# Optimization experiments

Measured on AMD Instinct MI355X. Metric: run time of the kernel, lower is better.

## Reference

```python
import jax, jax.numpy as jnp
import numpy as np

N = 20000
E = 320000
D = 512
H = 512


def _gcn_norm(edge_index, num_nodes):
    # PyG GCNConv: add self-loops, then sym-normalize with in-degree of A+I
    src = jnp.concatenate([edge_index[0], jnp.arange(num_nodes)])
    dst = jnp.concatenate([edge_index[1], jnp.arange(num_nodes)])
    deg = jax.ops.segment_sum(jnp.ones_like(dst, dtype=jnp.float32), dst, num_segments=num_nodes)
    dinv = jnp.where(deg > 0, jax.lax.rsqrt(deg), 0.0)
    norm = dinv[src] * dinv[dst]  # [E+N]
    return src, dst, norm


def _gcn_layer(x, src, dst, norm, W, b, num_nodes):
    h = x @ W                          # [N, out]
    msg = h[src] * norm[:, None]       # gather + scale, [E+N, out]
    out = jax.ops.segment_sum(msg, dst, num_segments=num_nodes)  # scatter-add
    return out + b


def setup_inputs() -> dict:
    key = jax.random.key(0)
    ks = jax.random.split(key, 8)
    features = jax.random.normal(ks[0], (N, D), dtype=jnp.float32)
    edge_index = jax.random.randint(ks[1], (2, E), 0, N, dtype=jnp.int64)
    edge_attr = jax.random.normal(ks[2], (E, 1), dtype=jnp.float32)  # unused by GCNConv
    s1 = 1.0 / np.sqrt(D)
    s2 = 1.0 / np.sqrt(H)
    W1 = jax.random.uniform(ks[3], (D, H), dtype=jnp.float32, minval=-s1, maxval=s1)
    b1 = jnp.zeros((H,), dtype=jnp.float32)
    W2 = jax.random.uniform(ks[4], (H, H), dtype=jnp.float32, minval=-s2, maxval=s2)
    b2 = jnp.zeros((H,), dtype=jnp.float32)
    return {"features": features, "edge_index": edge_index, "edge_attr": edge_attr,
            "W1": W1, "b1": b1, "W2": W2, "b2": b2}


def reference(features, edge_index, edge_attr, W1, b1, W2, b2):
    src, dst, norm = _gcn_norm(edge_index, N)
    x = jax.nn.relu(_gcn_layer(features, src, dst, norm, W1, b1, N))
    x = jax.nn.relu(_gcn_layer(x, src, dst, norm, W2, b2, N))
    # global_max_pool over the single graph (batch = all zeros) -> [1, H]
    return jnp.max(x, axis=0, keepdims=True)
```

## Files before the change

kernel.cpp:

```cpp
#include <hip/hip_runtime.h>

#define N_NODES 20000
#define MP      20096
#define N_EDGES 320000
#define DIM     512
#define SCAN_BLOCKS 79
#define FILL_BLOCKS 1250
#define CVT_BLOCKS  10048
#define W_BLOCKS    512
#define MAXP_BLOCKS 256
#define MAXP_ROWS   79

typedef _Float16 half8 __attribute__((ext_vector_type(8)));
typedef _Float16 half4v __attribute__((ext_vector_type(4)));
typedef _Float16 half2v __attribute__((ext_vector_type(2)));
typedef float floatx4 __attribute__((ext_vector_type(4)));

#define GLD16(g, l) __builtin_amdgcn_global_load_lds( \
    (const __attribute__((address_space(1))) unsigned int*)(g), \
    (__attribute__((address_space(3))) unsigned int*)(l), 16, 0, 0)

__global__ void k_count(const int* __restrict__ dst, int* __restrict__ cnt) {
    int e = blockIdx.x * blockDim.x + threadIdx.x;
    if (e < N_EDGES) atomicAdd(&cnt[dst[e]], 1);
}

__global__ __launch_bounds__(256) void k_scan_a(const int* __restrict__ cnt,
                                                int* __restrict__ bsum) {
    __shared__ int buf[256];
    int gi = blockIdx.x * 256 + threadIdx.x;
    buf[threadIdx.x] = (gi < N_NODES) ? cnt[gi] : 0;
    __syncthreads();
    for (int off = 128; off > 0; off >>= 1) {
        if (threadIdx.x < off) buf[threadIdx.x] += buf[threadIdx.x + off];
        __syncthreads();
    }
    if (threadIdx.x == 0) bsum[blockIdx.x] = buf[0];
}

__global__ __launch_bounds__(128) void k_scan_b(const int* __restrict__ bsum,
                                                int* __restrict__ bbase) {
    __shared__ int buf[128];
    int tid = threadIdx.x;
    int v = (tid < SCAN_BLOCKS) ? bsum[tid] : 0;
    buf[tid] = v;
    __syncthreads();
    for (int off = 1; off < 128; off <<= 1) {
        int t = (tid >= off) ? buf[tid - off] : 0;
        __syncthreads();
        buf[tid] += t;
        __syncthreads();
    }
    if (tid < SCAN_BLOCKS) bbase[tid] = buf[tid] - v;
}

__global__ __launch_bounds__(256) void k_scan_c(const int* __restrict__ cnt,
                                                const int* __restrict__ bbase,
                                                int* __restrict__ offs,
                                                int* __restrict__ cursor,
                                                float* __restrict__ dinv) {
    __shared__ int buf[256];
    int tid = threadIdx.x;
    int gi = blockIdx.x * 256 + tid;
    int v = (gi < N_NODES) ? cnt[gi] : 0;
    buf[tid] = v;
    __syncthreads();
    for (int off = 1; off < 256; off <<= 1) {
        int t = (tid >= off) ? buf[tid - off] : 0;
        __syncthreads();
        buf[tid] += t;
        __syncthreads();
    }
    int base = bbase[blockIdx.x];
    if (gi < N_NODES) {
        int incl = base + buf[tid];
        offs[gi + 1] = incl;
        cursor[gi] = incl - v;
        dinv[gi] = rsqrtf((float)v + 1.0f);
        if (gi == 0) offs[0] = 0;
    } else if (gi < MP) {
        dinv[gi] = 0.f;
    }
}

__global__ __launch_bounds__(256) void k_prep(const int* __restrict__ src,
                                              const int* __restrict__ dst,
                                              int* __restrict__ cursor,
                                              int* __restrict__ csr_src,
                                              const float* __restrict__ F,
                                              _Float16* __restrict__ A,
                                              const float* __restrict__ W1,
                                              const float* __restrict__ W2,
                                              _Float16* __restrict__ Wt1,
                                              _Float16* __restrict__ Wt2) {
    int b = blockIdx.x;
    if (b < FILL_BLOCKS) {
        int e = b * 256 + threadIdx.x;
        int d = dst[e];
        int pos = atomicAdd(&cursor[d], 1);
        csr_src[pos] = src[e];
        return;
    }
    if (b < FILL_BLOCKS + CVT_BLOCKS) {
        int i = (b - FILL_BLOCKS) * 256 + threadIdx.x;
        int e = i * 4;
        int row = e >> 9;
        half4v o;
        if (row < N_NODES) {
            float4 v = *(const float4*)&F[e];
            o[0] = (_Float16)v.x; o[1] = (_Float16)v.y;
            o[2] = (_Float16)v.z; o[3] = (_Float16)v.w;
        } else {
            o[0] = o[1] = o[2] = o[3] = (_Float16)0.f;
        }
        *(half4v*)&A[e] = o;
        return;
    }
    int local = b - (FILL_BLOCKS + CVT_BLOCKS);
    int z = local >> 8, t = local & 255;
    const float* W = z ? W2 : W1;
    _Float16* Wt = z ? Wt2 : Wt1;
    __shared__ float tile[32][33];
    int bx = (t & 15) * 32, by = (t >> 4) * 32;
    int x = threadIdx.x & 31, y4 = (threadIdx.x >> 5) * 4;
#pragma unroll
    for (int r = 0; r < 4; ++r)
        tile[y4 + r][x] = W[(size_t)(by + y4 + r) * DIM + bx + x];
    __syncthreads();
#pragma unroll
    for (int r = 0; r < 4; ++r)
        Wt[(size_t)(bx + y4 + r) * DIM + by + x] = (_Float16)tile[x][y4 + r];
}

__global__ __launch_bounds__(256) void k_gemm_f16(const _Float16* __restrict__ A,
                                                  const _Float16* __restrict__ Bt,
                                                  const float* __restrict__ dinv,
                                                  _Float16* __restrict__ G) {
    __shared__ _Float16 As[128 * 32];
    __shared__ _Float16 Bs[128 * 32];

    int t = threadIdx.x;
    int w = t >> 6, lane = t & 63;
    int lm = lane & 15, quad = lane >> 4;
    int m0 = blockIdx.x * 128, n0 = blockIdx.y * 128;
    int wm = (w & 1) * 64, wn = (w >> 1) * 64;

    floatx4 acc[4][4];
#pragma unroll
    for (int i = 0; i < 4; ++i)
#pragma unroll
        for (int j = 0; j < 4; ++j) acc[i][j] = (floatx4){0.f, 0.f, 0.f, 0.f};

    for (int k0 = 0; k0 < DIM; k0 += 32) {
        __syncthreads();
#pragma unroll
        for (int i = 0; i < 2; ++i) {
            int s = i * 256 + t;
            int m = s >> 2, kk = (s & 3) * 8;
            GLD16(A + (size_t)(m0 + m) * DIM + k0 + kk, As + s * 8);
            GLD16(Bt + (size_t)(n0 + m) * DIM + k0 + kk, Bs + s * 8);
        }
        __syncthreads();

        half8 af[4], bf[4];
#pragma unroll
        for (int i = 0; i < 4; ++i)
            af[i] = *(const half8*)&As[(wm + i * 16 + lm) * 32 + quad * 8];
#pragma unroll
        for (int j = 0; j < 4; ++j)
            bf[j] = *(const half8*)&Bs[(wn + j * 16 + lm) * 32 + quad * 8];
#pragma unroll
        for (int i = 0; i < 4; ++i)
#pragma unroll
            for (int j = 0; j < 4; ++j)
                acc[i][j] = __builtin_amdgcn_mfma_f32_16x16x32_f16(af[i], bf[j], acc[i][j], 0, 0, 0);
    }

#pragma unroll
    for (int i = 0; i < 4; ++i)
#pragma unroll
        for (int r = 0; r < 4; ++r) {
            int row = m0 + wm + i * 16 + quad * 4 + r;
            float dd = dinv[row];
#pragma unroll
            for (int j = 0; j < 4; ++j) {
                int col = n0 + wn + j * 16 + lm;
                G[(size_t)row * DIM + col] = (_Float16)(dd * acc[i][j][r]);
            }
        }
}

__global__ __launch_bounds__(256) void k_agg(const _Float16* __restrict__ g,
                                             const float* __restrict__ dinv,
                                             const int* __restrict__ offs,
                                             const int* __restrict__ csr_src,
                                             const float* __restrict__ bias,
                                             _Float16* __restrict__ out) {
    int node = blockIdx.x;
    if (node >= N_NODES) {
        ((unsigned int*)&out[(size_t)node * DIM])[threadIdx.x] = 0u;
        return;
    }
    __shared__ float part[4][DIM];
    int w = threadIdx.x >> 6, lane = threadIdx.x & 63;
    int f0 = lane * 8;

    float acc[8];
    if (w == 0) {
        half8 self = *(const half8*)&g[(size_t)node * DIM + f0];
#pragma unroll
        for (int i = 0; i < 8; ++i) acc[i] = (float)self[i];
    } else {
#pragma unroll
        for (int i = 0; i < 8; ++i) acc[i] = 0.f;
    }

    int beg = offs[node], end = offs[node + 1];
    int e = beg + w;
    for (; e + 12 < end; e += 16) {
        int s0 = csr_src[e], s1 = csr_src[e + 4], s2 = csr_src[e + 8], s3 = csr_src[e + 12];
        half8 v0 = *(const half8*)&g[(size_t)s0 * DIM + f0];
        half8 v1 = *(const half8*)&g[(size_t)s1 * DIM + f0];
        half8 v2 = *(const half8*)&g[(size_t)s2 * DIM + f0];
        half8 v3 = *(const half8*)&g[(size_t)s3 * DIM + f0];
#pragma unroll
        for (int i = 0; i < 8; ++i)
            acc[i] += ((float)v0[i] + (float)v1[i]) + ((float)v2[i] + (float)v3[i]);
    }
    for (; e < end; e += 4) {
        int s = csr_src[e];
        half8 v = *(const half8*)&g[(size_t)s * DIM + f0];
#pragma unroll
        for (int i = 0; i < 8; ++i) acc[i] += (float)v[i];
    }
#pragma unroll
    for (int i = 0; i < 8; ++i) part[w][f0 + i] = acc[i];
    __syncthreads();

    int f = threadIdx.x * 2;
    float dd = dinv[node];
    float s0 = part[0][f] + part[1][f] + part[2][f] + part[3][f];
    float s1 = part[0][f + 1] + part[1][f + 1] + part[2][f + 1] + part[3][f + 1];
    half2v o;
    o[0] = (_Float16)fmaxf(fmaf(dd, s0, bias[f]), 0.f);
    o[1] = (_Float16)fmaxf(fmaf(dd, s1, bias[f + 1]), 0.f);
    *(half2v*)&out[(size_t)node * DIM + f] = o;
}

__global__ __launch_bounds__(256) void k_maxpool(const _Float16* __restrict__ x,
                                                 float* __restrict__ out) {
    __shared__ float lmax[4][DIM];
    int stream = threadIdx.x >> 6, lane = threadIdx.x & 63;
    int f0 = lane * 8;
    int r0 = blockIdx.x * MAXP_ROWS;
    int r1 = min(r0 + MAXP_ROWS, N_NODES);

    float m[8];
#pragma unroll
    for (int i = 0; i < 8; ++i) m[i] = 0.f;
    for (int r = r0 + stream; r < r1; r += 4) {
        half8 v = *(const half8*)&x[(size_t)r * DIM + f0];
#pragma unroll
        for (int i = 0; i < 8; ++i) m[i] = fmaxf(m[i], (float)v[i]);
    }
#pragma unroll
    for (int i = 0; i < 8; ++i) lmax[stream][f0 + i] = m[i];
    __syncthreads();
#pragma unroll
    for (int rep = 0; rep < 2; ++rep) {
        int f = rep * 256 + threadIdx.x;
        float v = fmaxf(fmaxf(lmax[0][f], lmax[1][f]), fmaxf(lmax[2][f], lmax[3][f]));
        atomicMax((int*)&out[f], __float_as_int(v));
    }
}

extern "C" void kernel_launch(void* const* d_in, const int* in_sizes, int n_in,
                              void* d_out, int out_size, void* d_ws, size_t ws_size,
                              hipStream_t stream) {
    const float* features = (const float*)d_in[0];
    const int*   ei       = (const int*)d_in[1];
    const float* W1       = (const float*)d_in[3];
    const float* b1       = (const float*)d_in[4];
    const float* W2       = (const float*)d_in[5];
    const float* b2       = (const float*)d_in[6];
    float* out = (float*)d_out;

    const int* src = ei;
    const int* dst = ei + N_EDGES;

    char* p = (char*)d_ws;
    auto alloc = [&](size_t bytes) { void* r = p; p += (bytes + 255) & ~(size_t)255; return r; };
    int*      cnt    = (int*)alloc(N_NODES * 4);
    int*      offs   = (int*)alloc((N_NODES + 1) * 4);
    int*      cursor = (int*)alloc(N_NODES * 4);
    float*    dinv   = (float*)alloc(MP * 4);
    int*      csr    = (int*)alloc(N_EDGES * 4);
    int*      bsum   = (int*)alloc(SCAN_BLOCKS * 4);
    int*      bbase  = (int*)alloc(SCAN_BLOCKS * 4);
    _Float16* fA   = (_Float16*)alloc((size_t)MP * DIM * 2);
    _Float16* Wt1  = (_Float16*)alloc((size_t)DIM * DIM * 2);
    _Float16* Wt2  = (_Float16*)alloc((size_t)DIM * DIM * 2);
    _Float16* gbuf = (_Float16*)alloc((size_t)MP * DIM * 2);
    _Float16* x1f  = (_Float16*)alloc((size_t)MP * DIM * 2);
    _Float16* x2h  = (_Float16*)alloc((size_t)MP * DIM * 2);

    hipMemsetAsync(cnt, 0, N_NODES * 4, stream);
    hipMemsetAsync(out, 0, DIM * 4, stream);

    k_count<<<FILL_BLOCKS, 256, 0, stream>>>(dst, cnt);
    k_scan_a<<<SCAN_BLOCKS, 256, 0, stream>>>(cnt, bsum);
    k_scan_b<<<1, 128, 0, stream>>>(bsum, bbase);
    k_scan_c<<<SCAN_BLOCKS, 256, 0, stream>>>(cnt, bbase, offs, cursor, dinv);

    k_prep<<<FILL_BLOCKS + CVT_BLOCKS + W_BLOCKS, 256, 0, stream>>>(
        src, dst, cursor, csr, features, fA, W1, W2, Wt1, Wt2);

    dim3 ggrd(MP / 128, DIM / 128);

    k_gemm_f16<<<ggrd, 256, 0, stream>>>(fA, Wt1, dinv, gbuf);
    k_agg<<<MP, 256, 0, stream>>>(gbuf, dinv, offs, csr, b1, x1f);

    k_gemm_f16<<<ggrd, 256, 0, stream>>>(x1f, Wt2, dinv, gbuf);
    k_agg<<<N_NODES, 256, 0, stream>>>(gbuf, dinv, offs, csr, b2, x2h);

    k_maxpool<<<MAXP_BLOCKS, 256, 0, stream>>>(x2h, out);
}
```

Measured before the change: 281.4 us.

## Restructure aggregation: one wave per node per 64-feature chunk, shuffle reduction

Replaces the one-block-per-node aggregation with a mapping where each wavefront handles one node for a 64-feature chunk, and 8 lanes groups split the edges. Partial sums are combined with cross-lane xor shuffles instead of shared memory and __syncthreads, and bias/output use 8-wide vector accesses. This removes LDS traffic and block barriers and raises parallelism, but each gathered row access is now only 128 bytes per edge per wave and the explicit 4-way load unrolling is dropped, which may lower memory-level parallelism per lane.

```diff
diff --git a/kernel.cpp b/kernel.cpp
--- a/kernel.cpp
+++ b/kernel.cpp
@@ -13,7 +13,6 @@
 
 typedef _Float16 half8 __attribute__((ext_vector_type(8)));
 typedef _Float16 half4v __attribute__((ext_vector_type(4)));
-typedef _Float16 half2v __attribute__((ext_vector_type(2)));
 typedef float floatx4 __attribute__((ext_vector_type(4)));
 
 #define GLD16(g, l) __builtin_amdgcn_global_load_lds( \
@@ -190,24 +189,31 @@
         }
 }
 
-__global__ __launch_bounds__(256) void k_agg(const _Float16* __restrict__ g,
-                                             const float* __restrict__ dinv,
-                                             const int* __restrict__ offs,
-                                             const int* __restrict__ csr_src,
-                                             const float* __restrict__ bias,
-                                             _Float16* __restrict__ out) {
-    int node = blockIdx.x;
+__global__ __launch_bounds__(256) void k_agg_x(const _Float16* __restrict__ g,
+                                               const float* __restrict__ dinv,
+                                               const int* __restrict__ offs,
+                                               const int* __restrict__ csr_src,
+                                               const float* __restrict__ bias,
+                                               _Float16* __restrict__ out, int nodeCount) {
+    int chunk = blockIdx.x & 7;
+    int node = (blockIdx.x >> 3) * 4 + (threadIdx.x >> 6);
+    int lane = threadIdx.x & 63;
+    int slot = lane >> 3, fg = lane & 7;
+    int fbase = chunk * 64 + fg * 8;
+
     if (node >= N_NODES) {
-        ((unsigned int*)&out[(size_t)node * DIM])[threadIdx.x] = 0u;
+        if (node < nodeCount && slot == 0) {
+            half8 z;
+#pragma unroll
+            for (int i = 0; i < 8; ++i) z[i] = (_Float16)0.f;
+            *(half8*)&out[(size_t)node * DIM + fbase] = z;
+        }
         return;
     }
-    __shared__ float part[4][DIM];
-    int w = threadIdx.x >> 6, lane = threadIdx.x & 63;
-    int f0 = lane * 8;
 
     float acc[8];
-    if (w == 0) {
-        half8 self = *(const half8*)&g[(size_t)node * DIM + f0];
+    if (slot == 0) {
+        half8 self = *(const half8*)&g[(size_t)node * DIM + fbase];
 #pragma unroll
         for (int i = 0; i < 8; ++i) acc[i] = (float)self[i];
     } else {
@@ -216,35 +222,28 @@
     }
 
     int beg = offs[node], end = offs[node + 1];
-    int e = beg + w;
-    for (; e + 12 < end; e += 16) {
-        int s0 = csr_src[e], s1 = csr_src[e + 4], s2 = csr_src[e + 8], s3 = csr_src[e + 12];
-        half8 v0 = *(const half8*)&g[(size_t)s0 * DIM + f0];
-        half8 v1 = *(const half8*)&g[(size_t)s1 * DIM + f0];
-        half8 v2 = *(const half8*)&g[(size_t)s2 * DIM + f0];
-        half8 v3 = *(const half8*)&g[(size_t)s3 * DIM + f0];
-#pragma unroll
-        for (int i = 0; i < 8; ++i)
-            acc[i] += ((float)v0[i] + (float)v1[i]) + ((float)v2[i] + (float)v3[i]);
-    }
-    for (; e < end; e += 4) {
+    for (int e = beg + slot; e < end; e += 8) {
         int s = csr_src[e];
-        half8 v = *(const half8*)&g[(size_t)s * DIM + f0];
+        half8 v = *(const half8*)&g[(size_t)s * DIM + fbase];
 #pragma unroll
         for (int i = 0; i < 8; ++i) acc[i] += (float)v[i];
     }
-#pragma unroll
-    for (int i = 0; i < 8; ++i) part[w][f0 + i] = acc[i];
-    __syncthreads();
-
-    int f = threadIdx.x * 2;
-    float dd = dinv[node];
-    float s0 = part[0][f] + part[1][f] + part[2][f] + part[3][f];
-    float s1 = part[0][f + 1] + part[1][f + 1] + part[2][f + 1] + part[3][f + 1];
-    half2v o;
-    o[0] = (_Float16)fmaxf(fmaf(dd, s0, bias[f]), 0.f);
-    o[1] = (_Float16)fmaxf(fmaf(dd, s1, bias[f + 1]), 0.f);
-    *(half2v*)&out[(size_t)node * DIM + f] = o;
+
+#pragma unroll
+    for (int m = 8; m <= 32; m <<= 1)
+#pragma unroll
+        for (int i = 0; i < 8; ++i) acc[i] += __shfl_xor(acc[i], m, 64);
+
+    if (slot == 0) {
+        float dd = dinv[node];
+        float4 b0 = *(const float4*)&bias[fbase];
+        float4 b1 = *(const float4*)&bias[fbase + 4];
+        float bb[8] = {b0.x, b0.y, b0.z, b0.w, b1.x, b1.y, b1.z, b1.w};
+        half8 o;
+#pragma unroll
+        for (int i = 0; i < 8; ++i) o[i] = (_Float16)fmaxf(fmaf(dd, acc[i], bb[i]), 0.f);
+        *(half8*)&out[(size_t)node * DIM + fbase] = o;
+    }
 }
 
 __global__ __launch_bounds__(256) void k_maxpool(const _Float16* __restrict__ x,
@@ -318,10 +317,10 @@
     dim3 ggrd(MP / 128, DIM / 128);
 
     k_gemm_f16<<<ggrd, 256, 0, stream>>>(fA, Wt1, dinv, gbuf);
-    k_agg<<<MP, 256, 0, stream>>>(gbuf, dinv, offs, csr, b1, x1f);
+    k_agg_x<<<8 * (MP / 4), 256, 0, stream>>>(gbuf, dinv, offs, csr, b1, x1f, MP);
 
     k_gemm_f16<<<ggrd, 256, 0, stream>>>(x1f, Wt2, dinv, gbuf);
-    k_agg<<<N_NODES, 256, 0, stream>>>(gbuf, dinv, offs, csr, b2, x2h);
+    k_agg_x<<<8 * (N_NODES / 4), 256, 0, stream>>>(gbuf, dinv, offs, csr, b2, x2h, N_NODES);
 
     k_maxpool<<<MAXP_BLOCKS, 256, 0, stream>>>(x2h, out);
 }
```

Result: slower. 312.9 us (+11.2%).
